# Kernel optimization log

Measured on AMD Instinct MI355X. Metric: run time of the kernel, lower is better.

## Reference

```python
import jax, jax.numpy as jnp
import numpy as np

WINDOW = 2  # window_size

def _causal_window_conv(x, W, b):
    # x: [B,T,D_in], W: [WINDOW, D_in, D_out], b: [D_out]
    # equivalent to left-padding x by WINDOW-1 zeros and a 'valid' conv
    B, T, _ = x.shape
    xp = jnp.pad(x, ((0, 0), (WINDOW - 1, 0), (0, 0)))  # [B, T+WINDOW-1, D_in]
    out = b
    for k in range(WINDOW):
        out = out + jnp.einsum('btd,de->bte', xp[:, k:k + T], W[k])
    return out  # [B,T,D_out]

def setup_inputs() -> dict:
    key = jax.random.key(0)
    ks = jax.random.split(key, 4)
    B, T, Din, Dout = 8, 4096, 256, 256
    scale = 0.05
    x = jax.random.normal(ks[0], (B, T, Din), dtype=jnp.float32)
    W_z = jax.random.normal(ks[1], (WINDOW, Din, Dout), dtype=jnp.float32) * scale
    W_f = jax.random.normal(ks[2], (WINDOW, Din, Dout), dtype=jnp.float32) * scale
    W_o = jax.random.normal(ks[3], (WINDOW, Din, Dout), dtype=jnp.float32) * scale
    b_z = jnp.zeros((Dout,), dtype=jnp.float32)
    b_f = jnp.zeros((Dout,), dtype=jnp.float32)
    b_o = jnp.zeros((Dout,), dtype=jnp.float32)
    return {"x": x, "W_z": W_z, "W_f": W_f, "W_o": W_o,
            "b_z": b_z, "b_f": b_f, "b_o": b_o}

def reference(x, W_z, W_f, W_o, b_z, b_f, b_o):
    # QRNN with fo-pooling (Bradbury et al. 2016), return_sequences=True
    z = jnp.tanh(_causal_window_conv(x, W_z, b_z))          # [B,T,D]
    f = jax.nn.sigmoid(_causal_window_conv(x, W_f, b_f))    # [B,T,D]
    o = jax.nn.sigmoid(_causal_window_conv(x, W_o, b_o))    # [B,T,D]

    def step(c, zfo):
        z_t, f_t, o_t = zfo
        c = f_t * c + (1.0 - f_t) * z_t   # fo-pooling recurrence
        h = o_t * c
        return c, h

    c0 = jnp.zeros(z.shape[::2], dtype=z.dtype)  # [B,D]
    # time-major for scan
    zfo = (z.transpose(1, 0, 2), f.transpose(1, 0, 2), o.transpose(1, 0, 2))
    _, hs = jax.lax.scan(step, c0, zfo)
    return hs.transpose(1, 0, 2)  # [B,T,D]
```

## Files before the change

### kernel.cpp

```cpp
#include <hip/hip_runtime.h>
#include <hip/hip_bf16.h>
#include <hip/hip_fp16.h>

#define BDIM 8
#define TDIM 4096
#define DDIM 256
#define MDIM (BDIM * TDIM)
#define NCHUNK 256
#define LCHUNK (TDIM / NCHUNK)

typedef _Float16 f16x8 __attribute__((ext_vector_type(8)));
typedef _Float16 f16x4 __attribute__((ext_vector_type(4)));
typedef float f32x4 __attribute__((ext_vector_type(4)));

__device__ __forceinline__ float sigmoid_(float x) {
    return 1.0f / (1.0f + __expf(-x));
}
__device__ __forceinline__ float tanh_(float x) {
    return 2.0f / (1.0f + __expf(-2.0f * x)) - 1.0f;
}

#define GLOAD_LDS16(g, l)                                                    \
    __builtin_amdgcn_global_load_lds(                                        \
        (const __attribute__((address_space(1))) void*)(g),                  \
        (__attribute__((address_space(3))) void*)(l), 16, 0, 0)

__global__ __launch_bounds__(64) void convert_x(const float* __restrict__ x,
                                                _Float16* __restrict__ xpad) {
    const int tp = blockIdx.x;
    const int b = blockIdx.y;
    const int q = threadIdx.x;
    float4 v = make_float4(0.f, 0.f, 0.f, 0.f);
    if (tp > 0)
        v = *(const float4*)(x + ((size_t)b * TDIM + tp - 1) * DDIM + q * 4);
    f16x4 h;
    h[0] = (_Float16)v.x; h[1] = (_Float16)v.y;
    h[2] = (_Float16)v.z; h[3] = (_Float16)v.w;
    *(f16x4*)(xpad + ((size_t)b * (TDIM + 1) + tp) * DDIM + q * 4) = h;
}

__global__ __launch_bounds__(256) void convert_w(
    const float* __restrict__ Wz, const float* __restrict__ Wf,
    const float* __restrict__ Wo, _Float16* __restrict__ Wt) {
    const int idx = blockIdx.x * 256 + threadIdx.x;
    const int n = idx & 255;
    const int kin = (idx >> 8) & 255;
    const int w = (idx >> 16) & 1;
    const int g = idx >> 17;
    const float* W = (g == 0) ? Wz : (g == 1) ? Wf : Wo;
    const float v = W[(size_t)w * 65536 + (size_t)kin * 256 + n];
    Wt[((size_t)g * 256 + n) * 512 + w * 256 + kin] = (_Float16)v;
}

__global__ __launch_bounds__(256) void gates_mfma(
    const _Float16* __restrict__ xpad, const _Float16* __restrict__ Wt,
    const float* __restrict__ bz, const float* __restrict__ bfv,
    const float* __restrict__ bo,
    _Float16* __restrict__ zbuf, _Float16* __restrict__ fbuf,
    _Float16* __restrict__ obuf) {
    const int gate = blockIdx.z;
    const int m0 = blockIdx.x * 128;
    const int n0 = blockIdx.y * 128;
    const int tid = threadIdx.x;
    const int lane = tid & 63;
    const int wave = tid >> 6;
    const int wr = wave >> 1;
    const int wc = wave & 1;

    __shared__ __align__(16) char smem[49152];

    const int s = wave * 64 + lane;
    const int r1 = s >> 2;
    const int kc = (((s & 3) ^ ((s >> 3) & 3))) * 8;

    const int b = m0 >> 12;
    const int t0 = m0 & (TDIM - 1);

    const _Float16* srcA1 =
        xpad + ((size_t)b * (TDIM + 1) + t0 + r1) * DDIM + kc;
    const _Float16* srcA2 = srcA1 + (size_t)64 * DDIM;
    const _Float16* srcB1 = Wt + ((size_t)gate * 256 + n0 + r1) * 512 + kc;
    const _Float16* srcB2 = srcB1 + (size_t)64 * 512;

#define STAGE_(slot, t)                                                      \
    {                                                                        \
        char* dA = smem + (slot) * 16384 + wave * 1024;                      \
        char* dB = smem + (slot) * 16384 + 8192 + wave * 1024;               \
        GLOAD_LDS16(srcA1 + (t) * 32, dA);                                   \
        GLOAD_LDS16(srcA2 + (t) * 32, dA + 4096);                            \
        GLOAD_LDS16(srcB1 + (t) * 32, dB);                                   \
        GLOAD_LDS16(srcB2 + (t) * 32, dB + 4096);                            \
    }

    f32x4 acc[4][4] = {};
    const int am = lane & 15;
    const int kswz = (((lane >> 4) ^ ((lane >> 1) & 3))) * 8;

    STAGE_(0, 0);
    STAGE_(1, 1);

#pragma unroll
    for (int it = 0; it < 16; ++it) {
        if (it < 15)
            asm volatile("s_waitcnt vmcnt(4)" ::: "memory");
        else
            asm volatile("s_waitcnt vmcnt(0)" ::: "memory");
        __builtin_amdgcn_s_barrier();
        __builtin_amdgcn_sched_barrier(0);
        if (it < 14) STAGE_((it + 2) % 3, it + 2);
        __builtin_amdgcn_sched_barrier(0);

        const _Float16* Ab = (const _Float16*)(smem + (it % 3) * 16384);
        const _Float16* Bb = (const _Float16*)(smem + (it % 3) * 16384 + 8192);

        f16x8 a[4], bb[4];
#pragma unroll
        for (int i = 0; i < 4; ++i)
            a[i] = *(const f16x8*)(Ab + (wr * 64 + i * 16 + am) * 32 + kswz);
#pragma unroll
        for (int j = 0; j < 4; ++j)
            bb[j] = *(const f16x8*)(Bb + (wc * 64 + j * 16 + am) * 32 + kswz);

        asm volatile("s_waitcnt lgkmcnt(0)" ::: "memory");
        __builtin_amdgcn_sched_barrier(0);
        __builtin_amdgcn_s_setprio(1);
#pragma unroll
        for (int i = 0; i < 4; ++i)
#pragma unroll
            for (int j = 0; j < 4; ++j)
                acc[i][j] = __builtin_amdgcn_mfma_f32_16x16x32_f16(
                    a[i], bb[j], acc[i][j], 0, 0, 0);
        __builtin_amdgcn_s_setprio(0);
        __builtin_amdgcn_sched_barrier(0);
    }
#undef STAGE_

    __syncthreads();

    const float* bias = (gate == 0) ? bz : (gate == 1) ? bfv : bo;
    _Float16* outp = (gate == 0) ? zbuf : (gate == 1) ? fbuf : obuf;
    _Float16* eb = (_Float16*)smem + wave * 4608;
    const int rq = (lane >> 4) * 4;
#pragma unroll
    for (int j = 0; j < 4; ++j) {
        const int gc = n0 + wc * 64 + j * 16 + am;
        const float bj = bias[gc];
#pragma unroll
        for (int i = 0; i < 4; ++i) {
            f32x4 v = acc[i][j];
#pragma unroll
            for (int r = 0; r < 4; ++r) {
                const float val = v[r] + bj;
                const float act = (gate == 0) ? tanh_(val) : sigmoid_(val);
                eb[(i * 16 + rq + r) * 72 + j * 16 + am] = (_Float16)act;
            }
        }
    }
    __syncthreads();

    const int rrow = lane >> 3;
    const int rcol = (lane & 7) * 8;
#pragma unroll
    for (int rr = 0; rr < 8; ++rr) {
        const int row = rr * 8 + rrow;
        f16x8 v = *(const f16x8*)(eb + row * 72 + rcol);
        const size_t gm = (size_t)(m0 + wr * 64 + row);
        *(f16x8*)(outp + gm * DDIM + n0 + wc * 64 + rcol) = v;
    }
}

__global__ __launch_bounds__(256) void scan_pass1(
    const _Float16* __restrict__ zbuf, const _Float16* __restrict__ fbuf,
    float* __restrict__ aggA, float* __restrict__ aggB) {
    const int idx = blockIdx.x * 256 + threadIdx.x;
    const int d8 = idx & 31;
    const int chunk = (idx >> 5) & (NCHUNK - 1);
    const int b = idx >> 13;

    const size_t row0 = (size_t)b * TDIM + (size_t)chunk * LCHUNK;
    const int4* zp = (const int4*)zbuf + row0 * 32 + d8;
    const int4* fp = (const int4*)fbuf + row0 * 32 + d8;

    float A[8], c[8];
#pragma unroll
    for (int e = 0; e < 8; ++e) { A[e] = 1.0f; c[e] = 0.0f; }

    for (int i = 0; i < LCHUNK; ++i) {
        int4 fv = *fp;
        int4 zv = *zp;
        const _Float16* fh = (const _Float16*)&fv;
        const _Float16* zh = (const _Float16*)&zv;
#pragma unroll
        for (int e = 0; e < 8; ++e) {
            const float f = (float)fh[e];
            const float z = (float)zh[e];
            A[e] *= f;
            c[e] = f * c[e] + (1.0f - f) * z;
        }
        fp += 32;
        zp += 32;
    }
    ((float4*)aggA)[(size_t)idx * 2 + 0] = make_float4(A[0], A[1], A[2], A[3]);
    ((float4*)aggA)[(size_t)idx * 2 + 1] = make_float4(A[4], A[5], A[6], A[7]);
    ((float4*)aggB)[(size_t)idx * 2 + 0] = make_float4(c[0], c[1], c[2], c[3]);
    ((float4*)aggB)[(size_t)idx * 2 + 1] = make_float4(c[4], c[5], c[6], c[7]);
}

__global__ __launch_bounds__(256) void carry_scan(
    const float* __restrict__ aggA, const float* __restrict__ aggB,
    float* __restrict__ carry) {
    const int g = blockIdx.x * 256 + threadIdx.x;
    const int d = g & 255;
    const int b = g >> 8;
    const size_t base = (size_t)b * NCHUNK * 256 + d;

    float c = 0.0f;
    for (int ch0 = 0; ch0 < NCHUNK; ch0 += 8) {
        float A[8], Bv[8];
#pragma unroll
        for (int u = 0; u < 8; ++u) {
            const size_t p = base + (size_t)(ch0 + u) * 256;
            A[u] = aggA[p];
            Bv[u] = aggB[p];
        }
#pragma unroll
        for (int u = 0; u < 8; ++u) {
            const size_t p = base + (size_t)(ch0 + u) * 256;
            carry[p] = c;
            c = A[u] * c + Bv[u];
        }
    }
}

__global__ __launch_bounds__(256) void scan_pass2(
    const _Float16* __restrict__ zbuf, const _Float16* __restrict__ fbuf,
    const _Float16* __restrict__ obuf, const float* __restrict__ carry,
    float* __restrict__ out) {
    const int idx = blockIdx.x * 256 + threadIdx.x;
    const int d8 = idx & 31;
    const int chunk = (idx >> 5) & (NCHUNK - 1);
    const int b = idx >> 13;

    float c[8];
    float4 c0 = ((const float4*)carry)[(size_t)idx * 2];
    float4 c1 = ((const float4*)carry)[(size_t)idx * 2 + 1];
    c[0] = c0.x; c[1] = c0.y; c[2] = c0.z; c[3] = c0.w;
    c[4] = c1.x; c[5] = c1.y; c[6] = c1.z; c[7] = c1.w;

    const size_t row0 = (size_t)b * TDIM + (size_t)chunk * LCHUNK;
    const int4* zp = (const int4*)zbuf + row0 * 32 + d8;
    const int4* fp = (const int4*)fbuf + row0 * 32 + d8;
    const int4* op = (const int4*)obuf + row0 * 32 + d8;
    float4* hp = (float4*)out + row0 * 64 + d8 * 2;

    for (int i = 0; i < LCHUNK; ++i) {
        int4 fv = *fp;
        int4 zv = *zp;
        int4 ov = *op;
        const _Float16* fh = (const _Float16*)&fv;
        const _Float16* zh = (const _Float16*)&zv;
        const _Float16* oh = (const _Float16*)&ov;
        float h[8];
#pragma unroll
        for (int e = 0; e < 8; ++e) {
            const float f = (float)fh[e];
            const float z = (float)zh[e];
            c[e] = f * c[e] + (1.0f - f) * z;
            h[e] = (float)oh[e] * c[e];
        }
        hp[0] = make_float4(h[0], h[1], h[2], h[3]);
        hp[1] = make_float4(h[4], h[5], h[6], h[7]);
        fp += 32;
        zp += 32;
        op += 32;
        hp += 64;
    }
}

extern "C" void kernel_launch(void* const* d_in, const int* in_sizes, int n_in,
                              void* d_out, int out_size, void* d_ws,
                              size_t ws_size, hipStream_t stream) {
    const float* x = (const float*)d_in[0];
    const float* Wz = (const float*)d_in[1];
    const float* Wf = (const float*)d_in[2];
    const float* Wo = (const float*)d_in[3];
    const float* bz = (const float*)d_in[4];
    const float* bfv = (const float*)d_in[5];
    const float* bo = (const float*)d_in[6];
    float* out = (float*)d_out;

    char* p = (char*)d_ws;
    _Float16* xpad = (_Float16*)p;  p += (size_t)BDIM * (TDIM + 1) * DDIM * 2;
    _Float16* Wt = (_Float16*)p;    p += (size_t)3 * 256 * 512 * 2;
    _Float16* zbuf = (_Float16*)p;  p += (size_t)MDIM * DDIM * 2;
    _Float16* fbuf = (_Float16*)p;  p += (size_t)MDIM * DDIM * 2;
    _Float16* obuf = (_Float16*)p;  p += (size_t)MDIM * DDIM * 2;
    float* aggA = (float*)p;        p += (size_t)BDIM * NCHUNK * DDIM * 4;
    float* aggB = (float*)p;        p += (size_t)BDIM * NCHUNK * DDIM * 4;
    float* carry = (float*)p;

    convert_x<<<dim3(TDIM + 1, BDIM), 64, 0, stream>>>(x, xpad);
    convert_w<<<(3 * 2 * 256 * 256) / 256, 256, 0, stream>>>(Wz, Wf, Wo, Wt);

    gates_mfma<<<dim3(MDIM / 128, DDIM / 128, 3), 256, 0, stream>>>(
        xpad, Wt, bz, bfv, bo, zbuf, fbuf, obuf);

    scan_pass1<<<(BDIM * NCHUNK * 32) / 256, 256, 0, stream>>>(zbuf, fbuf,
                                                               aggA, aggB);
    carry_scan<<<(BDIM * DDIM) / 256, 256, 0, stream>>>(aggA, aggB, carry);
    scan_pass2<<<(BDIM * NCHUNK * 32) / 256, 256, 0, stream>>>(zbuf, fbuf,
                                                               obuf, carry, out);
}
```

Before: 173.4 us.

## Swap MFMA operands to write gates directly, widen conversion and scan threading

The MFMA operands are swapped so each lane holds four consecutive output columns. The epilogue can then add a float4 bias, apply the activation and store f16x4 straight to global memory, with no LDS staging and no two block barriers. Separately, convert_x processes four rows per 256-thread block instead of one row per 64-thread block, and both scan passes use 4 channels per thread instead of 8, doubling thread count to raise parallelism. The tradeoffs are narrower 8-byte global stores in the GEMM epilogue and smaller per-thread loads in the scans.

```diff
diff --git a/kernel.cpp b/kernel.cpp
--- a/kernel.cpp
+++ b/kernel.cpp
@@ -25,11 +25,12 @@
         (const __attribute__((address_space(1))) void*)(g),                  \
         (__attribute__((address_space(3))) void*)(l), 16, 0, 0)
 
-__global__ __launch_bounds__(64) void convert_x(const float* __restrict__ x,
-                                                _Float16* __restrict__ xpad) {
-    const int tp = blockIdx.x;
+__global__ __launch_bounds__(256) void convert_x(const float* __restrict__ x,
+                                                 _Float16* __restrict__ xpad) {
+    const int tp = blockIdx.x * 4 + (threadIdx.x >> 6);
     const int b = blockIdx.y;
-    const int q = threadIdx.x;
+    const int q = threadIdx.x & 63;
+    if (tp > TDIM) return;
     float4 v = make_float4(0.f, 0.f, 0.f, 0.f);
     if (tp > 0)
         v = *(const float4*)(x + ((size_t)b * TDIM + tp - 1) * DDIM + q * 4);
@@ -129,43 +130,37 @@
 #pragma unroll
             for (int j = 0; j < 4; ++j)
                 acc[i][j] = __builtin_amdgcn_mfma_f32_16x16x32_f16(
-                    a[i], bb[j], acc[i][j], 0, 0, 0);
+                    bb[j], a[i], acc[i][j], 0, 0, 0);
         __builtin_amdgcn_s_setprio(0);
         __builtin_amdgcn_sched_barrier(0);
     }
 #undef STAGE_
 
-    __syncthreads();
-
     const float* bias = (gate == 0) ? bz : (gate == 1) ? bfv : bo;
     _Float16* outp = (gate == 0) ? zbuf : (gate == 1) ? fbuf : obuf;
-    _Float16* eb = (_Float16*)smem + wave * 4608;
-    const int rq = (lane >> 4) * 4;
-#pragma unroll
-    for (int j = 0; j < 4; ++j) {
-        const int gc = n0 + wc * 64 + j * 16 + am;
-        const float bj = bias[gc];
-#pragma unroll
-        for (int i = 0; i < 4; ++i) {
+    const int nq = (lane >> 4) * 4;
+#pragma unroll
+    for (int i = 0; i < 4; ++i) {
+        const size_t gm = (size_t)(m0 + wr * 64 + i * 16 + am);
+#pragma unroll
+        for (int j = 0; j < 4; ++j) {
+            const int gc = n0 + wc * 64 + j * 16 + nq;
+            const float4 b4 = *(const float4*)(bias + gc);
             f32x4 v = acc[i][j];
-#pragma unroll
-            for (int r = 0; r < 4; ++r) {
-                const float val = v[r] + bj;
-                const float act = (gate == 0) ? tanh_(val) : sigmoid_(val);
-                eb[(i * 16 + rq + r) * 72 + j * 16 + am] = (_Float16)act;
+            f16x4 h;
+            if (gate == 0) {
+                h[0] = (_Float16)tanh_(v[0] + b4.x);
+                h[1] = (_Float16)tanh_(v[1] + b4.y);
+                h[2] = (_Float16)tanh_(v[2] + b4.z);
+                h[3] = (_Float16)tanh_(v[3] + b4.w);
+            } else {
+                h[0] = (_Float16)sigmoid_(v[0] + b4.x);
+                h[1] = (_Float16)sigmoid_(v[1] + b4.y);
+                h[2] = (_Float16)sigmoid_(v[2] + b4.z);
+                h[3] = (_Float16)sigmoid_(v[3] + b4.w);
             }
-        }
-    }
-    __syncthreads();
-
-    const int rrow = lane >> 3;
-    const int rcol = (lane & 7) * 8;
-#pragma unroll
-    for (int rr = 0; rr < 8; ++rr) {
-        const int row = rr * 8 + rrow;
-        f16x8 v = *(const f16x8*)(eb + row * 72 + rcol);
-        const size_t gm = (size_t)(m0 + wr * 64 + row);
-        *(f16x8*)(outp + gm * DDIM + n0 + wc * 64 + rcol) = v;
+            *(f16x4*)(outp + gm * DDIM + gc) = h;
+        }
     }
 }
 
@@ -173,37 +168,35 @@
     const _Float16* __restrict__ zbuf, const _Float16* __restrict__ fbuf,
     float* __restrict__ aggA, float* __restrict__ aggB) {
     const int idx = blockIdx.x * 256 + threadIdx.x;
-    const int d8 = idx & 31;
-    const int chunk = (idx >> 5) & (NCHUNK - 1);
-    const int b = idx >> 13;
+    const int d4 = idx & 63;
+    const int chunk = (idx >> 6) & (NCHUNK - 1);
+    const int b = idx >> 14;
 
     const size_t row0 = (size_t)b * TDIM + (size_t)chunk * LCHUNK;
-    const int4* zp = (const int4*)zbuf + row0 * 32 + d8;
-    const int4* fp = (const int4*)fbuf + row0 * 32 + d8;
-
-    float A[8], c[8];
-#pragma unroll
-    for (int e = 0; e < 8; ++e) { A[e] = 1.0f; c[e] = 0.0f; }
+    const int2* zp = (const int2*)zbuf + row0 * 64 + d4;
+    const int2* fp = (const int2*)fbuf + row0 * 64 + d4;
+
+    float A[4], c[4];
+#pragma unroll
+    for (int e = 0; e < 4; ++e) { A[e] = 1.0f; c[e] = 0.0f; }
 
     for (int i = 0; i < LCHUNK; ++i) {
-        int4 fv = *fp;
-        int4 zv = *zp;
+        int2 fv = *fp;
+        int2 zv = *zp;
         const _Float16* fh = (const _Float16*)&fv;
         const _Float16* zh = (const _Float16*)&zv;
 #pragma unroll
-        for (int e = 0; e < 8; ++e) {
+        for (int e = 0; e < 4; ++e) {
             const float f = (float)fh[e];
             const float z = (float)zh[e];
             A[e] *= f;
             c[e] = f * c[e] + (1.0f - f) * z;
         }
-        fp += 32;
-        zp += 32;
-    }
-    ((float4*)aggA)[(size_t)idx * 2 + 0] = make_float4(A[0], A[1], A[2], A[3]);
-    ((float4*)aggA)[(size_t)idx * 2 + 1] = make_float4(A[4], A[5], A[6], A[7]);
-    ((float4*)aggB)[(size_t)idx * 2 + 0] = make_float4(c[0], c[1], c[2], c[3]);
-    ((float4*)aggB)[(size_t)idx * 2 + 1] = make_float4(c[4], c[5], c[6], c[7]);
+        fp += 64;
+        zp += 64;
+    }
+    ((float4*)aggA)[idx] = make_float4(A[0], A[1], A[2], A[3]);
+    ((float4*)aggB)[idx] = make_float4(c[0], c[1], c[2], c[3]);
 }
 
 __global__ __launch_bounds__(256) void carry_scan(
@@ -237,42 +230,39 @@
     const _Float16* __restrict__ obuf, const float* __restrict__ carry,
     float* __restrict__ out) {
     const int idx = blockIdx.x * 256 + threadIdx.x;
-    const int d8 = idx & 31;
-    const int chunk = (idx >> 5) & (NCHUNK - 1);
-    const int b = idx >> 13;
-
-    float c[8];
-    float4 c0 = ((const float4*)carry)[(size_t)idx * 2];
-    float4 c1 = ((const float4*)carry)[(size_t)idx * 2 + 1];
+    const int d4 = idx & 63;
+    const int chunk = (idx >> 6) & (NCHUNK - 1);
+    const int b = idx >> 14;
+
+    float c[4];
+    const float4 c0 = ((const float4*)carry)[idx];
     c[0] = c0.x; c[1] = c0.y; c[2] = c0.z; c[3] = c0.w;
-    c[4] = c1.x; c[5] = c1.y; c[6] = c1.z; c[7] = c1.w;
 
     const size_t row0 = (size_t)b * TDIM + (size_t)chunk * LCHUNK;
-    const int4* zp = (const int4*)zbuf + row0 * 32 + d8;
-    const int4* fp = (const int4*)fbuf + row0 * 32 + d8;
-    const int4* op = (const int4*)obuf + row0 * 32 + d8;
-    float4* hp = (float4*)out + row0 * 64 + d8 * 2;
+    const int2* zp = (const int2*)zbuf + row0 * 64 + d4;
+    const int2* fp = (const int2*)fbuf + row0 * 64 + d4;
+    const int2* op = (const int2*)obuf + row0 * 64 + d4;
+    float4* hp = (float4*)out + row0 * 64 + d4;
 
     for (int i = 0; i < LCHUNK; ++i) {
-        int4 fv = *fp;
-        int4 zv = *zp;
-        int4 ov = *op;
+        int2 fv = *fp;
+        int2 zv = *zp;
+        int2 ov = *op;
         const _Float16* fh = (const _Float16*)&fv;
         const _Float16* zh = (const _Float16*)&zv;
         const _Float16* oh = (const _Float16*)&ov;
-        float h[8];
-#pragma unroll
-        for (int e = 0; e < 8; ++e) {
+        float h[4];
+#pragma unroll
+        for (int e = 0; e < 4; ++e) {
             const float f = (float)fh[e];
             const float z = (float)zh[e];
             c[e] = f * c[e] + (1.0f - f) * z;
             h[e] = (float)oh[e] * c[e];
         }
-        hp[0] = make_float4(h[0], h[1], h[2], h[3]);
-        hp[1] = make_float4(h[4], h[5], h[6], h[7]);
-        fp += 32;
-        zp += 32;
-        op += 32;
+        *hp = make_float4(h[0], h[1], h[2], h[3]);
+        fp += 64;
+        zp += 64;
+        op += 64;
         hp += 64;
     }
 }
@@ -299,15 +289,15 @@
     float* aggB = (float*)p;        p += (size_t)BDIM * NCHUNK * DDIM * 4;
     float* carry = (float*)p;
 
-    convert_x<<<dim3(TDIM + 1, BDIM), 64, 0, stream>>>(x, xpad);
+    convert_x<<<dim3((TDIM + 4) / 4, BDIM), 256, 0, stream>>>(x, xpad);
     convert_w<<<(3 * 2 * 256 * 256) / 256, 256, 0, stream>>>(Wz, Wf, Wo, Wt);
 
     gates_mfma<<<dim3(MDIM / 128, DDIM / 128, 3), 256, 0, stream>>>(
         xpad, Wt, bz, bfv, bo, zbuf, fbuf, obuf);
 
-    scan_pass1<<<(BDIM * NCHUNK * 32) / 256, 256, 0, stream>>>(zbuf, fbuf,
+    scan_pass1<<<(BDIM * NCHUNK * 64) / 256, 256, 0, stream>>>(zbuf, fbuf,
                                                                aggA, aggB);
     carry_scan<<<(BDIM * DDIM) / 256, 256, 0, stream>>>(aggA, aggB, carry);
-    scan_pass2<<<(BDIM * NCHUNK * 32) / 256, 256, 0, stream>>>(zbuf, fbuf,
+    scan_pass2<<<(BDIM * NCHUNK * 64) / 256, 256, 0, stream>>>(zbuf, fbuf,
                                                                obuf, carry, out);
 }
```

Result: no change. 171.0 us (-1.4%).
